# Kernel optimization log

Measured on AMD Instinct MI355X. Metric: run time of the kernel, lower is better.

The kernel has to match this reference:

```python
import jax, jax.numpy as jnp
import numpy as np

NUM_HEADS = 16
HEAD_DIM = 64
EMBED_DIM = 1024
NEG_INF = -1e9
LENGTHS = np.array([1024, 512, 768, 896, 1024, 640, 384, 896], dtype=np.int32)


def rotate_half(x):
    d = x.shape[-1] // 2
    return jnp.concatenate([-x[..., d:], x[..., :d]], axis=-1)


def setup_inputs() -> dict:
    key = jax.random.key(0)
    ks = jax.random.split(key, 8)
    E, H, Dh = EMBED_DIM, NUM_HEADS, HEAD_DIM
    T = int(LENGTHS.sum())  # 6144 packed tokens
    hidden_states = jax.random.normal(ks[0], (T, E), jnp.float32)
    # RoPE tables: positions restart at 0 for each packed segment
    pos = np.concatenate([np.arange(l) for l in LENGTHS]).astype(np.float32)
    inv_freq = 1.0 / (10000.0 ** (np.arange(0, Dh, 2, dtype=np.float32) / Dh))
    freqs = pos[:, None] * inv_freq[None, :]           # [T, Dh/2]
    emb = np.concatenate([freqs, freqs], axis=-1)       # [T, Dh]
    cos = jnp.asarray(np.cos(emb), jnp.float32)
    sin = jnp.asarray(np.sin(emb), jnp.float32)
    s = 0.02
    Wq = jax.random.normal(ks[1], (E, E), jnp.float32) * s
    Wk = jax.random.normal(ks[2], (E, E), jnp.float32) * s
    Wv = jax.random.normal(ks[3], (E, E), jnp.float32) * s
    Wo = jax.random.normal(ks[4], (E, E), jnp.float32) * s
    bq = jnp.zeros((E,), jnp.float32)
    bv = jnp.zeros((E,), jnp.float32)
    bo = jnp.zeros((E,), jnp.float32)
    return dict(hidden_states=hidden_states, seq_len=jnp.asarray(LENGTHS),
                cos=cos, sin=sin, Wq=Wq, bq=bq, Wk=Wk, Wv=Wv, bv=bv, Wo=Wo, bo=bo)


def reference(hidden_states, seq_len, cos, sin, Wq, bq, Wk, Wv, bv, Wo, bo):
    T, E = hidden_states.shape
    H, Dh = NUM_HEADS, HEAD_DIM
    # q/k/v projections (k_proj has no bias, matching nn.Linear(bias=False))
    q = (hidden_states @ Wq.T + bq).reshape(T, H, Dh)
    k = (hidden_states @ Wk.T).reshape(T, H, Dh)
    v = (hidden_states @ Wv.T + bv).reshape(T, H, Dh)
    # rotary embedding, cos/sin broadcast over heads
    c = cos[:, None, :]
    s = sin[:, None, :]
    q = q * c + rotate_half(q) * s
    k = k * c + rotate_half(k) * s
    # unpack ragged -> padded [B, Lmax, H, Dh] (indices are static wrt data)
    lens = np.asarray(seq_len)
    B = lens.shape[0]
    Lmax = int(lens.max())
    cu = np.concatenate([[0], np.cumsum(lens)])
    pad_idx = cu[:-1, None] + np.arange(Lmax)[None, :]   # [B, Lmax]
    valid = np.arange(Lmax)[None, :] < lens[:, None]     # [B, Lmax]
    pad_idx = np.where(valid, pad_idx, 0)
    qp = q[pad_idx]  # [B, Lmax, H, Dh]
    kp = k[pad_idx]
    vp = v[pad_idx]
    # attention with causal + key-padding mask (equivalent to per-segment loop)
    scores = jnp.einsum('bqhd,bkhd->bhqk', qp, kp) / np.sqrt(Dh).astype(np.float32)
    causal = np.tril(np.ones((Lmax, Lmax), dtype=bool))
    mask = causal[None, None, :, :] & valid[:, None, None, :]
    scores = jnp.where(mask, scores, NEG_INF)
    probs = jax.nn.softmax(scores, axis=-1)
    out = jnp.einsum('bhqk,bkhd->bqhd', probs, vp).reshape(B, Lmax, E)
    # repack padded -> [T, E]
    b_ids = np.repeat(np.arange(B), lens)
    l_ids = np.concatenate([np.arange(l) for l in lens])
    packed = out[b_ids, l_ids]
    return packed @ Wo.T + bo
```

## Files before the change

### kernel.cpp

```cpp
#include <hip/hip_runtime.h>
#include <stdint.h>

typedef __bf16 bf16;
typedef __bf16 bf16x8 __attribute__((ext_vector_type(8)));
typedef __bf16 bf16x4 __attribute__((ext_vector_type(4)));
typedef float f32x4 __attribute__((ext_vector_type(4)));

#define T_TOT 6144
#define E_DIM 1024
#define NHEAD 16

__device__ __forceinline__ void gload16(const void* g, void* l) {
    __builtin_amdgcn_global_load_lds((const __attribute__((address_space(1))) void*)g,
                                     (__attribute__((address_space(3))) void*)l, 16, 0, 0);
}

__global__ __launch_bounds__(256) void cvt_all_kernel(const float* __restrict__ hs,
        const float* __restrict__ wq, const float* __restrict__ wk,
        const float* __restrict__ wv, const float* __restrict__ wo,
        bf16* __restrict__ hsb, bf16* __restrict__ wqb, bf16* __restrict__ wkb,
        bf16* __restrict__ wvb, bf16* __restrict__ wob) {
    const size_t TE = (size_t)T_TOT * E_DIM;
    const size_t EE = (size_t)E_DIM * E_DIM;
    size_t i = ((size_t)blockIdx.x * 256 + threadIdx.x) * 4;
    const float* src; bf16* dst; size_t off;
    if (i < TE)               { src = hs; dst = hsb; off = i; }
    else if (i < TE + EE)     { src = wq; dst = wqb; off = i - TE; }
    else if (i < TE + 2 * EE) { src = wk; dst = wkb; off = i - TE - EE; }
    else if (i < TE + 3 * EE) { src = wv; dst = wvb; off = i - TE - 2 * EE; }
    else                      { src = wo; dst = wob; off = i - TE - 3 * EE; }
    float4 v = *reinterpret_cast<const float4*>(src + off);
    union { bf16 h[4]; uint2 u; } pk;
    pk.h[0] = (bf16)v.x; pk.h[1] = (bf16)v.y; pk.h[2] = (bf16)v.z; pk.h[3] = (bf16)v.w;
    *reinterpret_cast<uint2*>(dst + off) = pk.u;
}

__global__ __launch_bounds__(256, 2) void qkv_gemm_kernel(
        const bf16* __restrict__ hsb,
        const bf16* __restrict__ wq, const bf16* __restrict__ wk, const bf16* __restrict__ wv,
        const float* __restrict__ bq, const float* __restrict__ bv,
        const float* __restrict__ cosb, const float* __restrict__ sinb,
        bf16* __restrict__ qo, bf16* __restrict__ ko, bf16* __restrict__ vto) {
    __shared__ bf16 As[192 * 64];
    __shared__ bf16 Bs[128 * 64];

    const int b    = blockIdx.x;
    const int swzi = (b & 7) * 96 + (b >> 3);
    const int bn   = swzi & 7;
    const int t1   = swzi >> 3;
    const int bm   = t1 & 31;
    const int z    = t1 >> 5;
    const bf16*  W    = (z == 0) ? wq : (z == 1) ? wk : wv;
    const float* bias = (z == 0) ? bq : (z == 1) ? nullptr : bv;

    const int tid  = threadIdx.x;
    const int lane = tid & 63;
    const int wid  = tid >> 6;
    const int l15  = lane & 15, l4 = lane >> 4;
    const int wr   = wid >> 1, wc = wid & 1;

    f32x4 acc[6][4] = {};

    const bf16* Ag = hsb + (size_t)bm * 192 * E_DIM;
    const bf16* Bg = W   + (size_t)bn * 128 * E_DIM;

    const int srow = tid >> 3, sc8 = (tid & 7) * 8;

    for (int k0 = 0; k0 < E_DIM; k0 += 64) {
        #pragma unroll
        for (int j = 0; j < 6; ++j)
            gload16(Ag + (size_t)(j * 32 + srow) * E_DIM + k0 + sc8,
                    As + (size_t)(j * 256 + wid * 64) * 8);
        #pragma unroll
        for (int j = 0; j < 4; ++j)
            gload16(Bg + (size_t)(j * 32 + srow) * E_DIM + k0 + sc8,
                    Bs + (size_t)(j * 256 + wid * 64) * 8);
        __syncthreads();

        bf16x8 bfr[4][2];
        #pragma unroll
        for (int n = 0; n < 4; ++n)
            #pragma unroll
            for (int ks = 0; ks < 2; ++ks)
                bfr[n][ks] = *reinterpret_cast<const bf16x8*>(
                    &Bs[(wc * 64 + n * 16 + l15) * 64 + (ks * 4 + l4) * 8]);
        #pragma unroll
        for (int m = 0; m < 6; ++m) {
            bf16x8 af0 = *reinterpret_cast<const bf16x8*>(
                &As[(wr * 96 + m * 16 + l15) * 64 + l4 * 8]);
            bf16x8 af1 = *reinterpret_cast<const bf16x8*>(
                &As[(wr * 96 + m * 16 + l15) * 64 + (4 + l4) * 8]);
            #pragma unroll
            for (int n = 0; n < 4; ++n) {
                acc[m][n] = __builtin_amdgcn_mfma_f32_16x16x32_bf16(af0, bfr[n][0], acc[m][n], 0, 0, 0);
                acc[m][n] = __builtin_amdgcn_mfma_f32_16x16x32_bf16(af1, bfr[n][1], acc[m][n], 0, 0, 0);
            }
        }
        __syncthreads();
    }

    const int colb = bn * 128 + wc * 64;
    if (z <= 1) {
        bf16* out = (z == 0) ? qo : ko;
        #pragma unroll
        for (int n = 0; n < 2; ++n) {
            const int col_lo = colb + n * 16 + l15;
            const int dlo    = n * 16 + l15;
            const float b_lo = bias ? bias[col_lo] : 0.0f;
            const float b_hi = bias ? bias[col_lo + 32] : 0.0f;
            #pragma unroll
            for (int m = 0; m < 6; ++m) {
                #pragma unroll
                for (int r = 0; r < 4; ++r) {
                    const int t = bm * 192 + wr * 96 + m * 16 + l4 * 4 + r;
                    const float c = cosb[t * 64 + dlo];
                    const float s = sinb[t * 64 + dlo];
                    const float lo = acc[m][n][r] + b_lo;
                    const float hi = acc[m][n + 2][r] + b_hi;
                    out[(size_t)t * E_DIM + col_lo]      = (bf16)(lo * c - hi * s);
                    out[(size_t)t * E_DIM + col_lo + 32] = (bf16)(hi * c + lo * s);
                }
            }
        }
    } else {
        #pragma unroll
        for (int n = 0; n < 4; ++n) {
            const int col  = colb + n * 16 + l15;
            const float bc = bias[col];
            #pragma unroll
            for (int m = 0; m < 6; ++m) {
                const int t0r = bm * 192 + wr * 96 + m * 16 + l4 * 4;
                bf16x4 pk;
                #pragma unroll
                for (int r = 0; r < 4; ++r)
                    pk[r] = (bf16)(acc[m][n][r] + bc);
                *reinterpret_cast<bf16x4*>(vto + (size_t)col * T_TOT + t0r) = pk;
            }
        }
    }
}

__global__ __launch_bounds__(256, 4) void out_gemm_kernel(
        const bf16* __restrict__ attnb, const bf16* __restrict__ wo,
        const float* __restrict__ bo, float* __restrict__ out) {
    __shared__ bf16 As[64 * 64];
    __shared__ bf16 Bs[128 * 64];
    const int b   = blockIdx.x;
    const int swz = (b & 7) * 96 + (b >> 3);
    const int bn  = swz & 7;
    const int bm  = swz >> 3;

    const int tid  = threadIdx.x;
    const int lane = tid & 63;
    const int wid  = tid >> 6;
    const int l15  = lane & 15, l4 = lane >> 4;
    const int wr   = wid >> 1, wc = wid & 1;

    f32x4 acc[2][4] = {};

    const bf16* Ag = attnb + (size_t)bm * 64 * E_DIM;
    const bf16* Bg = wo    + (size_t)bn * 128 * E_DIM;

    const int srow = tid >> 3, sc8 = (tid & 7) * 8;

    for (int k0 = 0; k0 < E_DIM; k0 += 64) {
        #pragma unroll
        for (int j = 0; j < 2; ++j)
            gload16(Ag + (size_t)(j * 32 + srow) * E_DIM + k0 + sc8,
                    As + (size_t)(j * 256 + wid * 64) * 8);
        #pragma unroll
        for (int j = 0; j < 4; ++j)
            gload16(Bg + (size_t)(j * 32 + srow) * E_DIM + k0 + sc8,
                    Bs + (size_t)(j * 256 + wid * 64) * 8);
        __syncthreads();

        bf16x8 bfr[4][2];
        #pragma unroll
        for (int n = 0; n < 4; ++n)
            #pragma unroll
            for (int ks = 0; ks < 2; ++ks)
                bfr[n][ks] = *reinterpret_cast<const bf16x8*>(
                    &Bs[(wc * 64 + n * 16 + l15) * 64 + (ks * 4 + l4) * 8]);
        #pragma unroll
        for (int m = 0; m < 2; ++m) {
            bf16x8 af0 = *reinterpret_cast<const bf16x8*>(
                &As[(wr * 32 + m * 16 + l15) * 64 + l4 * 8]);
            bf16x8 af1 = *reinterpret_cast<const bf16x8*>(
                &As[(wr * 32 + m * 16 + l15) * 64 + (4 + l4) * 8]);
            #pragma unroll
            for (int n = 0; n < 4; ++n) {
                acc[m][n] = __builtin_amdgcn_mfma_f32_16x16x32_bf16(af0, bfr[n][0], acc[m][n], 0, 0, 0);
                acc[m][n] = __builtin_amdgcn_mfma_f32_16x16x32_bf16(af1, bfr[n][1], acc[m][n], 0, 0, 0);
            }
        }
        __syncthreads();
    }

    #pragma unroll
    for (int n = 0; n < 4; ++n) {
        const int col  = bn * 128 + wc * 64 + n * 16 + l15;
        const float bc = bo[col];
        #pragma unroll
        for (int m = 0; m < 2; ++m) {
            const int rowb = bm * 64 + wr * 32 + m * 16 + l4 * 4;
            #pragma unroll
            for (int r = 0; r < 4; ++r)
                out[(size_t)(rowb + r) * E_DIM + col] = acc[m][n][r] + bc;
        }
    }
}

__device__ __forceinline__ void stage_kv(const bf16* __restrict__ kp, const bf16* __restrict__ vtp,
                                         bf16* kls, bf16* vls, int tok0, int h,
                                         int wid, int lane) {
    #pragma unroll
    for (int j = 0; j < 2; ++j) {
        const int c   = j * 256 + wid * 64 + lane;
        const int row = c >> 3;
        const int c8s = (c & 7) ^ (row & 7);
        gload16(kp  + (size_t)(tok0 + row) * E_DIM + h * 64 + c8s * 8,
                kls + (size_t)(j * 256 + wid * 64) * 8);
        gload16(vtp + (size_t)(h * 64 + row) * T_TOT + tok0 + c8s * 8,
                vls + (size_t)(j * 256 + wid * 64) * 8);
    }
}

__device__ __forceinline__ int swz(int j, int col8) {
    return j * 64 + ((col8 ^ (j & 7)) << 3);
}

__global__ __launch_bounds__(256, 3) void attn_kernel(const bf16* __restrict__ q,
                                                      const bf16* __restrict__ k,
                                                      const bf16* __restrict__ vt,
                                                      bf16* __restrict__ attn) {
    const int cu[9] = {0, 1024, 1536, 2304, 3200, 4224, 4864, 5248, 6144};
    __shared__ bf16 kls[2][64 * 64];
    __shared__ bf16 vls[2][64 * 64];
    __shared__ bf16 p_lds[4][16][72];
    const int h   = blockIdx.x & 15;
    const int qt  = blockIdx.x >> 4;
    const int tid = threadIdx.x, lane = tid & 63, wid = tid >> 6;
    const int l15 = lane & 15, l4 = lane >> 4;

    const int tq0 = qt * 64;
    int b = 0;
    #pragma unroll
    for (int i = 0; i < 8; ++i) if (tq0 >= cu[i + 1]) b = i + 1;
    const int q0  = tq0 + wid * 16;
    const int p0  = q0 - cu[b];
    const int p0b = tq0 - cu[b];
    const int nkt = (p0b >> 6) + 1;
    const int pq  = p0 + l15;

    bf16x8 qf[2];
    #pragma unroll
    for (int kk = 0; kk < 2; ++kk) {
        bf16x8 raw = *reinterpret_cast<const bf16x8*>(
            q + (size_t)(q0 + l15) * E_DIM + h * 64 + kk * 32 + l4 * 8);
        #pragma unroll
        for (int e = 0; e < 8; ++e)
            qf[kk][e] = (bf16)((float)raw[e] * 0.125f);
    }

    f32x4 o[4] = {};
    float mcur = -1e30f, lcur = 0.0f;

    stage_kv(k, vt, kls[0], vls[0], cu[b], h, wid, lane);
    __syncthreads();

    for (int kt = 0; kt < nkt; ++kt) {
        const int cur = kt & 1;
        if (kt + 1 < nkt)
            stage_kv(k, vt, kls[cur ^ 1], vls[cur ^ 1], cu[b] + (kt + 1) * 64, h, wid, lane);

        const int j0 = kt * 64;
        const bool diag = (kt == nkt - 1);

        f32x4 s[4] = {};
        #pragma unroll
        for (int nt = 0; nt < 4; ++nt) {
            #pragma unroll
            for (int kk = 0; kk < 2; ++kk) {
                bf16x8 kf = *reinterpret_cast<const bf16x8*>(&kls[cur][swz(nt * 16 + l15, kk * 4 + l4)]);
                s[nt] = __builtin_amdgcn_mfma_f32_16x16x32_bf16(kf, qf[kk], s[nt], 0, 0, 0);
            }
        }

        float tmax = -1e30f;
        #pragma unroll
        for (int nt = 0; nt < 4; ++nt) {
            #pragma unroll
            for (int r = 0; r < 4; ++r) {
                float sv = s[nt][r];
                if (diag) {
                    const int kp = j0 + nt * 16 + l4 * 4 + r;
                    sv = (kp <= pq) ? sv : -1e30f;
                }
                s[nt][r] = sv;
                tmax = fmaxf(tmax, sv);
            }
        }
        tmax = fmaxf(tmax, __shfl_xor(tmax, 16));
        tmax = fmaxf(tmax, __shfl_xor(tmax, 32));

        if (!__all(tmax <= mcur + 8.0f)) {
            const float mnew  = fmaxf(mcur, tmax);
            const float alpha = __expf(mcur - mnew);
            #pragma unroll
            for (int nt = 0; nt < 4; ++nt)
                #pragma unroll
                for (int r = 0; r < 4; ++r) o[nt][r] *= alpha;
            lcur *= alpha;
            mcur = mnew;
        }

        float rs = 0.0f;
        #pragma unroll
        for (int nt = 0; nt < 4; ++nt) {
            bf16x4 pk;
            #pragma unroll
            for (int r = 0; r < 4; ++r) {
                float p = __expf(s[nt][r] - mcur);
                rs += p;
                pk[r] = (bf16)p;
            }
            *reinterpret_cast<bf16x4*>(&p_lds[wid][l15][nt * 16 + l4 * 4]) = pk;
        }
        rs += __shfl_xor(rs, 16);
        rs += __shfl_xor(rs, 32);
        lcur += rs;

        bf16x8 pf[2];
        #pragma unroll
        for (int kk = 0; kk < 2; ++kk)
            pf[kk] = *reinterpret_cast<const bf16x8*>(&p_lds[wid][l15][kk * 32 + l4 * 8]);

        #pragma unroll
        for (int nt = 0; nt < 4; ++nt) {
            #pragma unroll
            for (int kk = 0; kk < 2; ++kk) {
                bf16x8 vf = *reinterpret_cast<const bf16x8*>(&vls[cur][swz(nt * 16 + l15, kk * 4 + l4)]);
                o[nt] = __builtin_amdgcn_mfma_f32_16x16x32_bf16(vf, pf[kk], o[nt], 0, 0, 0);
            }
        }
        __syncthreads();
    }

    const float rinv = __builtin_amdgcn_rcpf(lcur);
    #pragma unroll
    for (int nt = 0; nt < 4; ++nt) {
        bf16x4 pk;
        #pragma unroll
        for (int r = 0; r < 4; ++r)
            pk[r] = (bf16)(o[nt][r] * rinv);
        *reinterpret_cast<bf16x4*>(
            attn + (size_t)(q0 + l15) * E_DIM + h * 64 + nt * 16 + l4 * 4) = pk;
    }
}

extern "C" void kernel_launch(void* const* d_in, const int* in_sizes, int n_in,
                              void* d_out, int out_size, void* d_ws, size_t ws_size,
                              hipStream_t stream) {
    const float* hs   = (const float*)d_in[0];
    const float* cosb = (const float*)d_in[2];
    const float* sinb = (const float*)d_in[3];
    const float* Wq   = (const float*)d_in[4];
    const float* bq   = (const float*)d_in[5];
    const float* Wk   = (const float*)d_in[6];
    const float* Wv   = (const float*)d_in[7];
    const float* bv   = (const float*)d_in[8];
    const float* Wo   = (const float*)d_in[9];
    const float* bo   = (const float*)d_in[10];

    const size_t TE = (size_t)T_TOT * E_DIM;
    const size_t EE = (size_t)E_DIM * E_DIM;

    char* w = (char*)d_ws;
    bf16* hsb   = (bf16*)w; w += TE * 2;
    bf16* wqb   = (bf16*)w; w += EE * 2;
    bf16* wkb   = (bf16*)w; w += EE * 2;
    bf16* wvb   = (bf16*)w; w += EE * 2;
    bf16* wob   = (bf16*)w; w += EE * 2;
    bf16* qb    = (bf16*)w; w += TE * 2;
    bf16* kb    = (bf16*)w; w += TE * 2;
    bf16* vtb   = (bf16*)w; w += TE * 2;
    bf16* attnb = (bf16*)w; w += TE * 2;

    const int cvt_blocks = (int)((TE + 4 * EE) / 4 / 256);
    cvt_all_kernel<<<cvt_blocks, 256, 0, stream>>>(hs, Wq, Wk, Wv, Wo, hsb, wqb, wkb, wvb, wob);

    qkv_gemm_kernel<<<768, 256, 0, stream>>>(hsb, wqb, wkb, wvb, bq, bv, cosb, sinb, qb, kb, vtb);

    attn_kernel<<<(T_TOT / 64) * NHEAD, 256, 0, stream>>>(qb, kb, vtb, attnb);

    out_gemm_kernel<<<768, 256, 0, stream>>>(attnb, wob, bo, (float*)d_out);
}
```

Before: 118.6 us.

## Triple-buffer LDS with async global-to-LDS prefetch in QKV and output GEMMs

Both projection GEMMs move from a single-buffered BK=64 loop with two __syncthreads per iteration to a three-stage ring of BK=32 LDS buffers. Tiles are prefetched two steps ahead with global_load_lds, and each step waits via an explicit vmcnt count plus a single scheduler-fenced barrier. The aim is to hide global load latency behind MFMA work and halve barrier count. In exchange there are twice as many k-iterations with less MFMA work each, and correctness relies on the hand-counted vmcnt values matching the number of outstanding loads.

```diff
diff --git a/kernel.cpp b/kernel.cpp
--- a/kernel.cpp
+++ b/kernel.cpp
@@ -14,6 +14,9 @@
     __builtin_amdgcn_global_load_lds((const __attribute__((address_space(1))) void*)g,
                                      (__attribute__((address_space(3))) void*)l, 16, 0, 0);
 }
+
+#define SBAR() do { __builtin_amdgcn_sched_barrier(0); __builtin_amdgcn_s_barrier(); \
+                    __builtin_amdgcn_sched_barrier(0); } while (0)
 
 __global__ __launch_bounds__(256) void cvt_all_kernel(const float* __restrict__ hs,
         const float* __restrict__ wq, const float* __restrict__ wk,
@@ -41,8 +44,8 @@
         const float* __restrict__ bq, const float* __restrict__ bv,
         const float* __restrict__ cosb, const float* __restrict__ sinb,
         bf16* __restrict__ qo, bf16* __restrict__ ko, bf16* __restrict__ vto) {
-    __shared__ bf16 As[192 * 64];
-    __shared__ bf16 Bs[128 * 64];
+    __shared__ bf16 As[3][192 * 32];
+    __shared__ bf16 Bs[3][128 * 32];
 
     const int b    = blockIdx.x;
     const int swzi = (b & 7) * 96 + (b >> 3);
@@ -64,39 +67,44 @@
     const bf16* Ag = hsb + (size_t)bm * 192 * E_DIM;
     const bf16* Bg = W   + (size_t)bn * 128 * E_DIM;
 
-    const int srow = tid >> 3, sc8 = (tid & 7) * 8;
-
-    for (int k0 = 0; k0 < E_DIM; k0 += 64) {
-        #pragma unroll
-        for (int j = 0; j < 6; ++j)
-            gload16(Ag + (size_t)(j * 32 + srow) * E_DIM + k0 + sc8,
-                    As + (size_t)(j * 256 + wid * 64) * 8);
-        #pragma unroll
-        for (int j = 0; j < 4; ++j)
-            gload16(Bg + (size_t)(j * 32 + srow) * E_DIM + k0 + sc8,
-                    Bs + (size_t)(j * 256 + wid * 64) * 8);
-        __syncthreads();
-
-        bf16x8 bfr[4][2];
+    const int srow = tid >> 2, sc4 = (tid & 3) * 8;
+
+    auto stage = [&](int k0, int buf) {
+        #pragma unroll
+        for (int j = 0; j < 3; ++j)
+            gload16(Ag + (size_t)(j * 64 + srow) * E_DIM + k0 + sc4,
+                    &As[buf][(j * 256 + wid * 64) * 8]);
+        #pragma unroll
+        for (int j = 0; j < 2; ++j)
+            gload16(Bg + (size_t)(j * 64 + srow) * E_DIM + k0 + sc4,
+                    &Bs[buf][(j * 256 + wid * 64) * 8]);
+    };
+
+    const int NT = E_DIM / 32;
+    stage(0, 0);
+    stage(32, 1);
+
+    for (int t = 0; t < NT; ++t) {
+        if (t < NT - 1) asm volatile("s_waitcnt vmcnt(5)" ::: "memory");
+        else            asm volatile("s_waitcnt vmcnt(0)" ::: "memory");
+        SBAR();
+        if (t + 2 < NT) stage((t + 2) * 32, (t + 2) % 3);
+
+        const bf16* Ab = As[t % 3];
+        const bf16* Bb = Bs[t % 3];
+        bf16x8 bfr[4];
         #pragma unroll
         for (int n = 0; n < 4; ++n)
-            #pragma unroll
-            for (int ks = 0; ks < 2; ++ks)
-                bfr[n][ks] = *reinterpret_cast<const bf16x8*>(
-                    &Bs[(wc * 64 + n * 16 + l15) * 64 + (ks * 4 + l4) * 8]);
+            bfr[n] = *reinterpret_cast<const bf16x8*>(
+                &Bb[(wc * 64 + n * 16 + l15) * 32 + l4 * 8]);
         #pragma unroll
         for (int m = 0; m < 6; ++m) {
-            bf16x8 af0 = *reinterpret_cast<const bf16x8*>(
-                &As[(wr * 96 + m * 16 + l15) * 64 + l4 * 8]);
-            bf16x8 af1 = *reinterpret_cast<const bf16x8*>(
-                &As[(wr * 96 + m * 16 + l15) * 64 + (4 + l4) * 8]);
-            #pragma unroll
-            for (int n = 0; n < 4; ++n) {
-                acc[m][n] = __builtin_amdgcn_mfma_f32_16x16x32_bf16(af0, bfr[n][0], acc[m][n], 0, 0, 0);
-                acc[m][n] = __builtin_amdgcn_mfma_f32_16x16x32_bf16(af1, bfr[n][1], acc[m][n], 0, 0, 0);
-            }
-        }
-        __syncthreads();
+            bf16x8 af = *reinterpret_cast<const bf16x8*>(
+                &Ab[(wr * 96 + m * 16 + l15) * 32 + l4 * 8]);
+            #pragma unroll
+            for (int n = 0; n < 4; ++n)
+                acc[m][n] = __builtin_amdgcn_mfma_f32_16x16x32_bf16(af, bfr[n], acc[m][n], 0, 0, 0);
+        }
     }
 
     const int colb = bn * 128 + wc * 64;
@@ -143,8 +151,8 @@
 __global__ __launch_bounds__(256, 4) void out_gemm_kernel(
         const bf16* __restrict__ attnb, const bf16* __restrict__ wo,
         const float* __restrict__ bo, float* __restrict__ out) {
-    __shared__ bf16 As[64 * 64];
-    __shared__ bf16 Bs[128 * 64];
+    __shared__ bf16 As[3][64 * 32];
+    __shared__ bf16 Bs[3][128 * 32];
     const int b   = blockIdx.x;
     const int swz = (b & 7) * 96 + (b >> 3);
     const int bn  = swz & 7;
@@ -161,39 +169,41 @@
     const bf16* Ag = attnb + (size_t)bm * 64 * E_DIM;
     const bf16* Bg = wo    + (size_t)bn * 128 * E_DIM;
 
-    const int srow = tid >> 3, sc8 = (tid & 7) * 8;
-
-    for (int k0 = 0; k0 < E_DIM; k0 += 64) {
+    const int srow = tid >> 2, sc4 = (tid & 3) * 8;
+
+    auto stage = [&](int k0, int buf) {
+        gload16(Ag + (size_t)srow * E_DIM + k0 + sc4, &As[buf][(wid * 64) * 8]);
         #pragma unroll
         for (int j = 0; j < 2; ++j)
-            gload16(Ag + (size_t)(j * 32 + srow) * E_DIM + k0 + sc8,
-                    As + (size_t)(j * 256 + wid * 64) * 8);
-        #pragma unroll
-        for (int j = 0; j < 4; ++j)
-            gload16(Bg + (size_t)(j * 32 + srow) * E_DIM + k0 + sc8,
-                    Bs + (size_t)(j * 256 + wid * 64) * 8);
-        __syncthreads();
-
-        bf16x8 bfr[4][2];
+            gload16(Bg + (size_t)(j * 64 + srow) * E_DIM + k0 + sc4,
+                    &Bs[buf][(j * 256 + wid * 64) * 8]);
+    };
+
+    const int NT = E_DIM / 32;
+    stage(0, 0);
+    stage(32, 1);
+
+    for (int t = 0; t < NT; ++t) {
+        if (t < NT - 1) asm volatile("s_waitcnt vmcnt(3)" ::: "memory");
+        else            asm volatile("s_waitcnt vmcnt(0)" ::: "memory");
+        SBAR();
+        if (t + 2 < NT) stage((t + 2) * 32, (t + 2) % 3);
+
+        const bf16* Ab = As[t % 3];
+        const bf16* Bb = Bs[t % 3];
+        bf16x8 bfr[4];
         #pragma unroll
         for (int n = 0; n < 4; ++n)
-            #pragma unroll
-            for (int ks = 0; ks < 2; ++ks)
-                bfr[n][ks] = *reinterpret_cast<const bf16x8*>(
-                    &Bs[(wc * 64 + n * 16 + l15) * 64 + (ks * 4 + l4) * 8]);
+            bfr[n] = *reinterpret_cast<const bf16x8*>(
+                &Bb[(wc * 64 + n * 16 + l15) * 32 + l4 * 8]);
         #pragma unroll
         for (int m = 0; m < 2; ++m) {
-            bf16x8 af0 = *reinterpret_cast<const bf16x8*>(
-                &As[(wr * 32 + m * 16 + l15) * 64 + l4 * 8]);
-            bf16x8 af1 = *reinterpret_cast<const bf16x8*>(
-                &As[(wr * 32 + m * 16 + l15) * 64 + (4 + l4) * 8]);
-            #pragma unroll
-            for (int n = 0; n < 4; ++n) {
-                acc[m][n] = __builtin_amdgcn_mfma_f32_16x16x32_bf16(af0, bfr[n][0], acc[m][n], 0, 0, 0);
-                acc[m][n] = __builtin_amdgcn_mfma_f32_16x16x32_bf16(af1, bfr[n][1], acc[m][n], 0, 0, 0);
-            }
-        }
-        __syncthreads();
+            bf16x8 af = *reinterpret_cast<const bf16x8*>(
+                &Ab[(wr * 32 + m * 16 + l15) * 32 + l4 * 8]);
+            #pragma unroll
+            for (int n = 0; n < 4; ++n)
+                acc[m][n] = __builtin_amdgcn_mfma_f32_16x16x32_bf16(af, bfr[n], acc[m][n], 0, 0, 0);
+        }
     }
 
     #pragma unroll
```

After: 146.2 us. 1.23x slower.
